# Optimization experiments

Measured on AMD Instinct MI355X. Metric: run time of the kernel, lower is better.

## Reference

```python
import jax, jax.numpy as jnp
import numpy as np
from jax import lax

# Kernel / geometry constants matching init_kwargs
KZ, KX, KY = 9, 15, 15          # PSF support
STRIDE = (1, 1, 1)              # scale = (zscale, xscale, yscale)
Z_PAD = (KZ - 1 + 1) // 2       # 4
X_PAD = (KX - 1 + 1) // 2       # 7
Y_PAD = (KY - 1 + 1) // 2       # 7


def _dist(n):
    # |idx - n//2|, matching _distance_from_center
    return jnp.abs(jnp.arange(n, dtype=jnp.float32) - n // 2)


def gen_psf(bet_xy, bet_z, alpha):
    b = bet_xy.shape[0]
    zd = _dist(KZ)                                  # [KZ]
    xd = _dist(KX)
    yd = _dist(KY)
    # gen_distance_plane: dp[i, j] = xd[j]^2 + yd[i]^2  (shape [KY, KX])
    dp = yd[:, None] ** 2 + xd[None, :] ** 2
    # gen_2dnorm: [b, KY, KX]
    bxy = bet_xy[:, None, None]
    lat = jnp.exp(-dp[None] / (2.0 * bxy ** 2)) / (2.0 * jnp.pi * bxy ** 2)
    # gen_1dnorm: [b, KZ]
    bz = bet_z[:, None]
    ax = jnp.exp(-(zd[None] ** 2) / (2.0 * bz ** 2)) / (jnp.sqrt(2.0 * jnp.pi) * bz)
    # psf = exp(log(lateral) + log(axial)) == lateral * axial  -> [b, 1, KZ, KY, KX]
    psf = lat[:, None, None, :, :] * ax[:, None, :, None, None]
    # double_exp mode
    psf = 1.0 - jnp.exp(-alpha[:, None, None, None, None] * psf)
    return psf / jnp.sum(psf)


def reference(x, bet_xy, bet_z, alpha):
    # x: [B, 1, Z, X, Y]; original computes dense conv3d giving [B, B, ...] and
    # keeps only the diagonal _x[b, b]. That is mathematically a per-sample
    # (grouped) convolution, implemented here without the O(B) redundancy.
    psf = gen_psf(bet_xy, bet_z, alpha)             # [B, 1, KZ, KY, KX]
    B = x.shape[0]
    xin = jnp.transpose(x, (1, 0, 2, 3, 4))         # [1, B, Z, X, Y]
    out = lax.conv_general_dilated(
        xin, psf,
        window_strides=STRIDE,
        padding=[(Z_PAD, Z_PAD), (X_PAD, X_PAD), (Y_PAD, Y_PAD)],
        dimension_numbers=("NCDHW", "OIDHW", "NCDHW"),
        feature_group_count=B,
    )                                               # [1, B, Z', X', Y']
    return jnp.transpose(out, (1, 0, 2, 3, 4))      # [B, 1, Z', X', Y']


def setup_inputs() -> dict:
    key = jax.random.key(0)
    k1, k2, k3, k4 = jax.random.split(key, 4)
    B = 4
    x = jax.random.normal(k1, (B, 1, 32, 192, 192), dtype=jnp.float32)
    bet_xy = 1.0 + 2.0 * jax.random.uniform(k2, (B,), dtype=jnp.float32)   # in [1, 3)
    bet_z = 1.0 + 2.0 * jax.random.uniform(k3, (B,), dtype=jnp.float32)    # in [1, 3)
    alpha = 1.0 + 9.0 * jax.random.uniform(k4, (B,), dtype=jnp.float32)    # in [1, 10)
    return {"x": x, "bet_xy": bet_xy, "bet_z": bet_z, "alpha": alpha}
```

## Files before the change

### kernel.cpp

```cpp
#include <hip/hip_runtime.h>
#include <math.h>

#define B_ 4
#define D_ 32
#define H_ 192
#define W_ 192
#define HW_ (H_ * W_)

#define NT 5

#define TW 48
#define TH 12
#define NTHR 256
#define ZCHUNK 16
#define NP (ZCHUNK + 8)

#define XT_H 26
#define XT_COLS 62
#define XT_W 72
#define XT_CELLS (XT_H * XT_COLS)
#define NSEC 7

#define R_S 48
#define R_H 26

#define XT_SZ (XT_H * XT_W)
#define SMEM_WORDS (2 * XT_SZ + 2 * NT * R_H * R_S)

#define NTAPS (B_ * 9 * 15 * 15)

__device__ inline float4 f4fma(float c, float4 a, float4 d) {
    d.x = fmaf(c, a.x, d.x); d.y = fmaf(c, a.y, d.y);
    d.z = fmaf(c, a.z, d.z); d.w = fmaf(c, a.w, d.w);
    return d;
}
__device__ inline float4 f4add(float4 a, float4 b) {
    a.x += b.x; a.y += b.y; a.z += b.z; a.w += b.w; return a;
}
__device__ inline float rfl(float x) {
    return __int_as_float(__builtin_amdgcn_readfirstlane(__float_as_int(x)));
}

__global__ __launch_bounds__(NTHR)
void conv_kernel(const float* __restrict__ x,
                 const float* __restrict__ bet_xy,
                 const float* __restrict__ bet_z,
                 const float* __restrict__ alpha,
                 float* __restrict__ out) {
    __shared__ __align__(16) float smem[SMEM_WORDS];
    float* xtb = smem;
    float* Rb  = smem + 2 * XT_SZ;
    float* red = smem;
    float* ct  = smem + 512;

    const int t  = threadIdx.x;
    const int w0 = blockIdx.x * TW;
    const int h0 = blockIdx.y * TH;
    const int bz = blockIdx.z;
    const int b  = bz & 3;
    const int z0 = (bz >> 2) * ZCHUNK;
    const float INV = 0.3989422804014327f;

    float local = 0.f;
#pragma unroll
    for (int s = 0; s < 32; ++s) {
        int idx = t + s * NTHR;
        if (idx < NTAPS) {
            int bb = idx / 2025;
            int r  = idx % 2025;
            int dz = r / 225;
            int r2 = r % 225;
            int dh = r2 / 15;
            int dw = r2 % 15;
            float bxy = bet_xy[bb], bzv = bet_z[bb], al = alpha[bb];
            float zd = (float)(dz - 4), hd = (float)(dh - 7), wd = (float)(dw - 7);
            float az = expf(-zd * zd / (2.f * bzv * bzv)) * (INV / bzv);
            float gh = expf(-hd * hd / (2.f * bxy * bxy)) * (INV / bxy);
            float gw = expf(-wd * wd / (2.f * bxy * bxy)) * (INV / bxy);
            local += 1.f - expf(-al * az * gh * gw);
        }
    }
    red[t] = local;
    __syncthreads();
    for (int s = 128; s > 0; s >>= 1) {
        if (t < s) red[t] += red[t + s];
        __syncthreads();
    }
    const float S = red[0];
    __syncthreads();

    if (t < NT * 13) {
        int n = t / 13;
        int k = t % 13;
        float bxy = bet_xy[b], bzv = bet_z[b], al = alpha[b];
        if (k < 8) {
            float d = (float)k;
            float g = expf(-d * d / (2.f * bxy * bxy)) * (INV / bxy);
            float p = g;
            for (int q = 0; q < n; ++q) p *= g;
            ct[n * 16 + k] = p;
        } else {
            float d = (float)(k - 8);
            float az = expf(-d * d / (2.f * bzv * bzv)) * (INV / bzv);
            float base = al * az;
            float p = base;
            for (int q = 0; q < n; ++q) p *= base;
            const float facs[NT] = {1.f, 2.f, 6.f, 24.f, 120.f};
            float sign = (n & 1) ? -1.f : 1.f;
            ct[n * 16 + k] = sign * p / (facs[n] * S);
        }
    }
    __syncthreads();

    float cg_[NT][8], cz_[NT][5];
#pragma unroll
    for (int n = 0; n < NT; ++n) {
#pragma unroll
        for (int k = 0; k < 8; ++k) cg_[n][k] = rfl(ct[n * 16 + k]);
#pragma unroll
        for (int k = 0; k < 5; ++k) cz_[n][k] = rfl(ct[n * 16 + 8 + k]);
    }
    __syncthreads();

    const float* xb = x + (size_t)b * (D_ * HW_);
    int goff[NSEC], loff[NSEC];
#pragma unroll
    for (int k = 0; k < NSEC; ++k) {
        int i = t + k * NTHR;
        int r = i / XT_COLS, c = i - r * XT_COLS;
        int gh = h0 + r - 7, gw = w0 + c - 7;
        bool ok = (i < XT_CELLS) && gh >= 0 && gh < H_ && gw >= 0 && gw < W_;
        goff[k] = ok ? (gh * W_ + gw) : -1;
        loff[k] = (i < XT_CELLS) ? (r * XT_W + c) : (XT_SZ - 1);
    }
    {
        int zi0 = z0 - 4;
        if (zi0 >= 0) {
#pragma unroll
            for (int k = 0; k < NSEC; ++k) {
                float v = 0.f;
                if (goff[k] >= 0) v = xb[(size_t)zi0 * HW_ + goff[k]];
                xtb[loff[k]] = v;
            }
        }
    }

    const int i0r = t / 12,  i0c = t - 12 * i0r;
    const int i1  = t + 56;
    const int i1r = i1 / 12, i1c = i1 - 12 * i1r;
    const bool sec1 = (t >= 200);
    const int wb0 = i0r * XT_W + 4 * i0c, rw0 = i0r * R_S + 4 * i0c;
    const int wb1 = i1r * XT_W + 4 * i1c, rw1 = i1r * R_S + 4 * i1c;
    const bool hact = (t < TH * 12);
    const int ro = t / 12, cgh = t - 12 * ro;
    const int hb = ro * R_S + 4 * cgh;

    float4 acc[9];
#pragma unroll
    for (int k = 0; k < 9; ++k) acc[k] = make_float4(0.f, 0.f, 0.f, 0.f);

#pragma unroll 1
    for (int p = 0; p <= NP; ++p) {
        __syncthreads();

        const int zi = z0 - 4 + p;
        const bool do_w  = (p < NP) && (zi >= 0) && (zi < D_);
        const int  zn    = zi + 1;
        const bool pvalid = (p + 1 < NP) && (zn >= 0) && (zn < D_);

        float pv[NSEC];
        if (pvalid) {
            const float* xp = xb + (size_t)zn * HW_;
#pragma unroll
            for (int k = 0; k < NSEC; ++k) pv[k] = (goff[k] >= 0) ? xp[goff[k]] : 0.f;
        }

        if (do_w) {
            const float* xt = xtb + (p & 1) * XT_SZ;
            float* Rw = Rb + (p & 1) * (NT * R_H * R_S);
#pragma unroll
            for (int sec = 0; sec < 2; ++sec) {
                if (sec == 1 && !sec1) break;
                const int wb = sec ? wb1 : wb0;
                const int rw = sec ? rw1 : rw0;
                float win[20];
                {
                    const float4* p4 = (const float4*)&xt[wb];
#pragma unroll
                    for (int q = 0; q < 5; ++q) {
                        float4 a = p4[q];
                        win[4 * q] = a.x; win[4 * q + 1] = a.y;
                        win[4 * q + 2] = a.z; win[4 * q + 3] = a.w;
                    }
                }
                float cj[4], sp[4][7];
#pragma unroll
                for (int j = 0; j < 4; ++j) {
                    cj[j] = win[j + 7];
#pragma unroll
                    for (int k = 1; k <= 7; ++k) sp[j][k - 1] = win[j + 7 - k] + win[j + 7 + k];
                }
#pragma unroll
                for (int n = 0; n < NT; ++n) {
                    float4 a;
                    a.x = cg_[n][0] * cj[0]; a.y = cg_[n][0] * cj[1];
                    a.z = cg_[n][0] * cj[2]; a.w = cg_[n][0] * cj[3];
#pragma unroll
                    for (int k = 1; k <= 7; ++k) {
                        float c = cg_[n][k];
                        a.x = fmaf(c, sp[0][k - 1], a.x);
                        a.y = fmaf(c, sp[1][k - 1], a.y);
                        a.z = fmaf(c, sp[2][k - 1], a.z);
                        a.w = fmaf(c, sp[3][k - 1], a.w);
                    }
                    *(float4*)&Rw[n * (R_H * R_S) + rw] = a;
                }
            }
        }

        if (p >= 1) {
            const int ziq = zi - 1;
            if (hact) {
                if (ziq >= 0 && ziq < D_) {
                    const float* Rr = Rb + ((p - 1) & 1) * (NT * R_H * R_S);
#pragma unroll
                    for (int n = 0; n < NT; ++n) {
                        const float* R1 = Rr + n * (R_H * R_S);
                        float4 rv[15];
#pragma unroll
                        for (int dh = 0; dh < 15; ++dh)
                            rv[dh] = *(const float4*)&R1[hb + dh * R_S];
                        float4 q;
                        q.x = cg_[n][0] * rv[7].x; q.y = cg_[n][0] * rv[7].y;
                        q.z = cg_[n][0] * rv[7].z; q.w = cg_[n][0] * rv[7].w;
#pragma unroll
                        for (int k = 1; k <= 7; ++k)
                            q = f4fma(cg_[n][k], f4add(rv[7 - k], rv[7 + k]), q);
                        acc[4] = f4fma(cz_[n][0], q, acc[4]);
#pragma unroll
                        for (int j = 1; j <= 4; ++j) {
                            float cz = cz_[n][j];
                            acc[4 + j] = f4fma(cz, q, acc[4 + j]);
                            acc[4 - j] = f4fma(cz, q, acc[4 - j]);
                        }
                    }
                }
                if (p - 1 >= 8) {
                    int z = z0 + (p - 1 - 8);
                    size_t o = ((size_t)(b * D_ + z) * H_ + (h0 + ro)) * W_ + (w0 + 4 * cgh);
                    *(float4*)&out[o] = acc[0];
                }
#pragma unroll
                for (int k = 0; k < 8; ++k) acc[k] = acc[k + 1];
                acc[8] = make_float4(0.f, 0.f, 0.f, 0.f);
            }
        }

        if (pvalid) {
            float* xn = xtb + ((p + 1) & 1) * XT_SZ;
#pragma unroll
            for (int k = 0; k < NSEC; ++k) xn[loff[k]] = pv[k];
        }
    }
}

extern "C" void kernel_launch(void* const* d_in, const int* in_sizes, int n_in,
                              void* d_out, int out_size, void* d_ws, size_t ws_size,
                              hipStream_t stream) {
    const float* x      = (const float*)d_in[0];
    const float* bet_xy = (const float*)d_in[1];
    const float* bet_z  = (const float*)d_in[2];
    const float* alpha  = (const float*)d_in[3];
    float* out = (float*)d_out;

    hipLaunchKernelGGL(conv_kernel, dim3(W_ / TW, H_ / TH, B_ * (D_ / ZCHUNK)),
                       dim3(NTHR), 0, stream, x, bet_xy, bet_z, alpha, out);
}
```

Before: 156.3 us.

## Swap separable pass order: vertical pass first, horizontal pass from LDS rows

The separable 2D Gaussian stage now runs the vertical (H) filter first from the input tile into a narrower 12-row intermediate buffer, then the horizontal (W) filter reads contiguous 20-float windows from that buffer. This shrinks the intermediate LDS buffer and cuts the first-stage work from 26 rows to 12 rows, using 192 of 256 threads instead of two sections. It also rotates thread-to-work assignment per block to spread idle threads across SIMDs. The horizontal pass now needs more LDS reads per output row and a different padded stride, which may change bank-conflict behaviour.

New measurement: 171.2 us. 9.6% more time.

```diff
diff --git a/kernel.cpp b/kernel.cpp
--- a/kernel.cpp
+++ b/kernel.cpp
@@ -20,12 +20,14 @@
 #define XT_W 72
 #define XT_CELLS (XT_H * XT_COLS)
 #define NSEC 7
-
-#define R_S 48
-#define R_H 26
-
 #define XT_SZ (XT_H * XT_W)
-#define SMEM_WORDS (2 * XT_SZ + 2 * NT * R_H * R_S)
+
+#define R2_H 12
+#define R2_S 68
+#define R2_PL (R2_H * R2_S)
+#define RBUF (NT * R2_PL)
+
+#define SMEM_WORDS (2 * XT_SZ + 2 * RBUF)
 
 #define NTAPS (B_ * 9 * 15 * 15)
 
@@ -145,15 +147,15 @@
         }
     }
 
-    const int i0r = t / 12,  i0c = t - 12 * i0r;
-    const int i1  = t + 56;
-    const int i1r = i1 / 12, i1c = i1 - 12 * i1r;
-    const bool sec1 = (t >= 200);
-    const int wb0 = i0r * XT_W + 4 * i0c, rw0 = i0r * R_S + 4 * i0c;
-    const int wb1 = i1r * XT_W + 4 * i1c, rw1 = i1r * R_S + 4 * i1c;
-    const bool hact = (t < TH * 12);
-    const int ro = t / 12, cgh = t - 12 * ro;
-    const int hb = ro * R_S + 4 * cgh;
+    const int bid = blockIdx.x + (int)gridDim.x * (blockIdx.y + (int)gridDim.y * blockIdx.z);
+    const int rt  = (t + ((bid >> 8) << 6)) & (NTHR - 1);
+
+    const int s1r = rt >> 4, s1c = rt & 15;
+    const int s1x = s1r * XT_W + 4 * s1c;
+    const int s1w = s1r * R2_S + 4 * s1c;
+    const bool s2act = (rt < TH * 12);
+    const int s2ro = rt / 12, s2cg = rt - 12 * s2ro;
+    const int s2r  = s2ro * R2_S + 4 * s2cg;
 
     float4 acc[9];
 #pragma unroll
@@ -164,7 +166,7 @@
         __syncthreads();
 
         const int zi = z0 - 4 + p;
-        const bool do_w  = (p < NP) && (zi >= 0) && (zi < D_);
+        const bool do_s1 = (p < NP) && (zi >= 0) && (zi < D_) && (rt < 192);
         const int  zn    = zi + 1;
         const bool pvalid = (p + 1 < NP) && (zn >= 0) && (zn < D_);
 
@@ -175,85 +177,72 @@
             for (int k = 0; k < NSEC; ++k) pv[k] = (goff[k] >= 0) ? xp[goff[k]] : 0.f;
         }
 
-        if (do_w) {
+        if (do_s1) {
             const float* xt = xtb + (p & 1) * XT_SZ;
-            float* Rw = Rb + (p & 1) * (NT * R_H * R_S);
-#pragma unroll
-            for (int sec = 0; sec < 2; ++sec) {
-                if (sec == 1 && !sec1) break;
-                const int wb = sec ? wb1 : wb0;
-                const int rw = sec ? rw1 : rw0;
-                float win[20];
-                {
-                    const float4* p4 = (const float4*)&xt[wb];
-#pragma unroll
-                    for (int q = 0; q < 5; ++q) {
-                        float4 a = p4[q];
-                        win[4 * q] = a.x; win[4 * q + 1] = a.y;
-                        win[4 * q + 2] = a.z; win[4 * q + 3] = a.w;
+            float* Rw = Rb + (p & 1) * RBUF + s1w;
+            float4 ctr = *(const float4*)&xt[s1x + 7 * XT_W];
+            float4 sp[7];
+#pragma unroll
+            for (int k = 1; k <= 7; ++k) {
+                float4 a  = *(const float4*)&xt[s1x + (7 - k) * XT_W];
+                float4 b2 = *(const float4*)&xt[s1x + (7 + k) * XT_W];
+                sp[k - 1] = f4add(a, b2);
+            }
+#pragma unroll
+            for (int n = 0; n < NT; ++n) {
+                float c0 = cg_[n][0];
+                float4 a;
+                a.x = c0 * ctr.x; a.y = c0 * ctr.y;
+                a.z = c0 * ctr.z; a.w = c0 * ctr.w;
+#pragma unroll
+                for (int k = 1; k <= 7; ++k) a = f4fma(cg_[n][k], sp[k - 1], a);
+                *(float4*)&Rw[n * R2_PL] = a;
+            }
+        }
+
+        if (p >= 1 && s2act) {
+            const int ziq = zi - 1;
+            if (ziq >= 0 && ziq < D_) {
+                const float* Rr = Rb + ((p - 1) & 1) * RBUF + s2r;
+#pragma unroll
+                for (int n = 0; n < NT; ++n) {
+                    const float* R1 = Rr + n * R2_PL;
+                    float win[20];
+#pragma unroll
+                    for (int q5 = 0; q5 < 5; ++q5) {
+                        float4 a = *(const float4*)&R1[4 * q5];
+                        win[4 * q5]     = a.x; win[4 * q5 + 1] = a.y;
+                        win[4 * q5 + 2] = a.z; win[4 * q5 + 3] = a.w;
+                    }
+                    float c0 = cg_[n][0];
+                    float4 qv;
+                    qv.x = c0 * win[7];  qv.y = c0 * win[8];
+                    qv.z = c0 * win[9];  qv.w = c0 * win[10];
+#pragma unroll
+                    for (int k = 1; k <= 7; ++k) {
+                        float c = cg_[n][k];
+                        qv.x = fmaf(c, win[7 - k]  + win[7 + k],  qv.x);
+                        qv.y = fmaf(c, win[8 - k]  + win[8 + k],  qv.y);
+                        qv.z = fmaf(c, win[9 - k]  + win[9 + k],  qv.z);
+                        qv.w = fmaf(c, win[10 - k] + win[10 + k], qv.w);
+                    }
+                    acc[4] = f4fma(cz_[n][0], qv, acc[4]);
+#pragma unroll
+                    for (int j = 1; j <= 4; ++j) {
+                        float cz = cz_[n][j];
+                        acc[4 + j] = f4fma(cz, qv, acc[4 + j]);
+                        acc[4 - j] = f4fma(cz, qv, acc[4 - j]);
                     }
                 }
-                float cj[4], sp[4][7];
-#pragma unroll
-                for (int j = 0; j < 4; ++j) {
-                    cj[j] = win[j + 7];
-#pragma unroll
-                    for (int k = 1; k <= 7; ++k) sp[j][k - 1] = win[j + 7 - k] + win[j + 7 + k];
-                }
-#pragma unroll
-                for (int n = 0; n < NT; ++n) {
-                    float4 a;
-                    a.x = cg_[n][0] * cj[0]; a.y = cg_[n][0] * cj[1];
-                    a.z = cg_[n][0] * cj[2]; a.w = cg_[n][0] * cj[3];
-#pragma unroll
-                    for (int k = 1; k <= 7; ++k) {
-                        float c = cg_[n][k];
-                        a.x = fmaf(c, sp[0][k - 1], a.x);
-                        a.y = fmaf(c, sp[1][k - 1], a.y);
-                        a.z = fmaf(c, sp[2][k - 1], a.z);
-                        a.w = fmaf(c, sp[3][k - 1], a.w);
-                    }
-                    *(float4*)&Rw[n * (R_H * R_S) + rw] = a;
-                }
-            }
-        }
-
-        if (p >= 1) {
-            const int ziq = zi - 1;
-            if (hact) {
-                if (ziq >= 0 && ziq < D_) {
-                    const float* Rr = Rb + ((p - 1) & 1) * (NT * R_H * R_S);
-#pragma unroll
-                    for (int n = 0; n < NT; ++n) {
-                        const float* R1 = Rr + n * (R_H * R_S);
-                        float4 rv[15];
-#pragma unroll
-                        for (int dh = 0; dh < 15; ++dh)
-                            rv[dh] = *(const float4*)&R1[hb + dh * R_S];
-                        float4 q;
-                        q.x = cg_[n][0] * rv[7].x; q.y = cg_[n][0] * rv[7].y;
-                        q.z = cg_[n][0] * rv[7].z; q.w = cg_[n][0] * rv[7].w;
-#pragma unroll
-                        for (int k = 1; k <= 7; ++k)
-                            q = f4fma(cg_[n][k], f4add(rv[7 - k], rv[7 + k]), q);
-                        acc[4] = f4fma(cz_[n][0], q, acc[4]);
-#pragma unroll
-                        for (int j = 1; j <= 4; ++j) {
-                            float cz = cz_[n][j];
-                            acc[4 + j] = f4fma(cz, q, acc[4 + j]);
-                            acc[4 - j] = f4fma(cz, q, acc[4 - j]);
-                        }
-                    }
-                }
-                if (p - 1 >= 8) {
-                    int z = z0 + (p - 1 - 8);
-                    size_t o = ((size_t)(b * D_ + z) * H_ + (h0 + ro)) * W_ + (w0 + 4 * cgh);
-                    *(float4*)&out[o] = acc[0];
-                }
-#pragma unroll
-                for (int k = 0; k < 8; ++k) acc[k] = acc[k + 1];
-                acc[8] = make_float4(0.f, 0.f, 0.f, 0.f);
-            }
+            }
+            if (p - 1 >= 8) {
+                int z = z0 + (p - 1 - 8);
+                size_t o = ((size_t)(b * D_ + z) * H_ + (h0 + s2ro)) * W_ + (w0 + 4 * s2cg);
+                *(float4*)&out[o] = acc[0];
+            }
+#pragma unroll
+            for (int k = 0; k < 8; ++k) acc[k] = acc[k + 1];
+            acc[8] = make_float4(0.f, 0.f, 0.f, 0.f);
         }
 
         if (pvalid) {
```
